# Kernel optimization log

Measured on AMD Instinct MI355X. Metric: run time of the kernel, lower is better.

Reference implementation:

```python
import jax, jax.numpy as jnp
import numpy as np

N, T, D = 2, 4096, 1024
H, E, L = 8, 4, 32
DK, DV = 64, 64

def setup_inputs():
    key = jax.random.key(0)
    ks = jax.random.split(key, 8)
    def randw(k, *d):
        return jax.random.normal(k, d, dtype=jnp.float32) / np.float32(np.sqrt(d[-1]))
    return {
        "X": jax.random.normal(ks[0], (N, T, D), dtype=jnp.float32),
        "w_G": randw(ks[1], H, E, D),
        "b_G": jnp.full((H, E), -float(H) ** 0.5, dtype=jnp.float32),
        "w_K": randw(ks[2], H, DK, D),
        "w_V": randw(ks[3], H, DV, D),
        "w_Q": randw(ks[4], H, DK, D),
        "w_O": randw(ks[5], DV * H, D),
        "init_K_rec": randw(ks[6], E, L, DK),
        "init_V_rec": randw(ks[7], E, L, DV),
    }

def _pscan(A, Xv, Y0):
    # Y_t = A_t * Y_{t-1} + X_t along axis 3 (chunk index), Y_{-1} = Y0
    Ae = jnp.broadcast_to(A[..., None], Xv.shape)
    Xv = Xv.at[..., 0, :].add(A[..., 0, None] * Y0)
    def op(c1, c2):
        a1, x1 = c1
        a2, x2 = c2
        return a1 * a2, a2 * x1 + x2
    _, Y = jax.lax.associative_scan(op, (Ae, Xv), axis=3)
    return Y

def reference(X, w_G, b_G, w_K, w_V, w_Q, w_O, init_K_rec, init_V_rec):
    n, t, _ = X.shape
    t_pad = ((t - 1) // L + 1) * L
    Xp = jnp.pad(X, ((0, 0), (0, t_pad - t), (0, 0)))
    # gates and projections
    G = jax.nn.sigmoid(jnp.einsum('ntd,hed->nhet', Xp, w_G) + b_G[None, :, :, None])
    K = jnp.einsum('ntc,hdc->nhtd', Xp, w_K)
    V = jnp.einsum('ntc,hdc->nhtd', Xp, w_V)
    A = 1.0 - jnp.minimum(G.sum(axis=1), 1.0)               # [n, E, t_pad]
    gK = jnp.einsum('nhet,nhtd->netd', G, K)
    gV = jnp.einsum('nhet,nhtd->netd', G, V)
    # split time as (L, t_pad//L): outer dim L, scan over chunk index (matches torch unflatten(2,(L,-1)))
    tc = t_pad // L
    A = A.reshape(n, E, L, tc)
    gK = gK.reshape(n, E, L, tc, DK)
    gV = gV.reshape(n, E, L, tc, DV)
    iK = jnp.broadcast_to(init_K_rec[None], (n, E, L, DK))
    iV = jnp.broadcast_to(init_V_rec[None], (n, E, L, DV))
    nK = _pscan(A, gK, iK).reshape(n, E, t_pad, DK)
    nV = _pscan(A, gV, iV).reshape(n, E, t_pad, DV)
    recK = jnp.concatenate([iK, nK], axis=2)                 # [n, E, L+t_pad, DK]
    recV = jnp.concatenate([iV, nV], axis=2)
    # moving window of size L ending at current position (slice starts at index 1 of rec buffer)
    idx = 1 + jnp.arange(t_pad)[:, None] + jnp.arange(L)[None, :]
    uk = recK[:, :, idx]                                     # [n, E, t_pad, L, DK]
    uv = recV[:, :, idx]                                     # [n, E, t_pad, L, DV]
    Q = jnp.einsum('ntc,hdc->nhtd', Xp, w_Q)
    scores = jnp.einsum('nhtd,netld->nhtel', Q, uk) / jnp.float32(np.sqrt(DK))
    probs = jax.nn.softmax(scores.reshape(n, H, t_pad, E * L), axis=-1).reshape(scores.shape)
    Y = jnp.einsum('nhtel,netld->nthd', probs, uv).reshape(n, t_pad, H * DV)
    return (Y @ w_O)[:, :t]
```

## Files before the change

### kernel.cpp

```cpp
#include <hip/hip_runtime.h>
#include <hip/hip_bf16.h>


using f4 = float4;
typedef __attribute__((ext_vector_type(8))) short short8;
typedef __attribute__((ext_vector_type(4))) float floatx4;

__device__ __forceinline__ ushort f2bf(float x) {
  unsigned u = __float_as_uint(x);
  u += 0x7fffu + ((u >> 16) & 1u);
  return (ushort)(u >> 16);
}
__device__ __forceinline__ unsigned pk2(float lo, float hi) {
  return (unsigned)f2bf(lo) | ((unsigned)f2bf(hi) << 16);
}
__device__ __forceinline__ float bflo(unsigned pk) { return __uint_as_float(pk << 16); }
__device__ __forceinline__ float bfhi(unsigned pk) { return __uint_as_float(pk & 0xffff0000u); }

__device__ __forceinline__ void gll16(const void* g, void* l) {
  __builtin_amdgcn_global_load_lds((const __attribute__((address_space(1))) void*)g,
                                   (__attribute__((address_space(3))) void*)l, 16, 0, 0);
}

__global__ __launch_bounds__(256)
void conv_f32_bf16(const float* __restrict__ src, ushort* __restrict__ dst, int n4) {
  for (int i = blockIdx.x * blockDim.x + threadIdx.x; i < n4; i += gridDim.x * blockDim.x) {
    f4 v = ((const f4*)src)[i];
    ushort4 o; o.x = f2bf(v.x); o.y = f2bf(v.y); o.z = f2bf(v.z); o.w = f2bf(v.w);
    ((ushort4*)dst)[i] = o;
  }
}

__global__ __launch_bounds__(256)
void conv_weights(const float* __restrict__ wK, const float* __restrict__ wV,
                  const float* __restrict__ wQ, const float* __restrict__ wG,
                  ushort* __restrict__ wAll) {
  int i4 = blockIdx.x * 256 + threadIdx.x;
  int idx = i4 * 4;
  int row = idx >> 10;
  f4 v = make_float4(0.f, 0.f, 0.f, 0.f);
  if (row < 512)       v = *(const f4*)&wK[idx];
  else if (row < 1024) v = *(const f4*)&wV[idx - 524288];
  else if (row < 1536) v = *(const f4*)&wQ[idx - 1048576];
  else if (row < 1568) v = *(const f4*)&wG[idx - 1572864];
  ushort4 o; o.x = f2bf(v.x); o.y = f2bf(v.y); o.z = f2bf(v.z); o.w = f2bf(v.w);
  *(ushort4*)&wAll[idx] = o;
}

__global__ __launch_bounds__(256)
void transpose_wO(const float* __restrict__ wO, ushort* __restrict__ wObf) {
  int i = blockIdx.x * 256 + threadIdx.x;
  int n = i >> 9, k = i & 511;
  wObf[i] = f2bf(wO[(size_t)k * 1024 + n]);
}

__global__ __launch_bounds__(256)
void proj_gemm_mfma(const ushort* __restrict__ Xbf, const ushort* __restrict__ wAll,
                    float* __restrict__ Kp, float* __restrict__ Vp,
                    float* __restrict__ Qp, float* __restrict__ Glin)
{
  __shared__ ushort As[4096];
  __shared__ ushort Bs[4096];
  const int tid = threadIdx.x;
  const int m0 = blockIdx.y * 128;
  const int ct = blockIdx.x;

  float* C; int Nc, n0;
  if (ct < 12) {
    int which = ct >> 2;
    C = (which == 0) ? Kp : (which == 1) ? Vp : Qp;
    Nc = 512; n0 = (ct & 3) * 128;
  } else { C = Glin; Nc = 32; n0 = 0; }

  const int lane = tid & 63;
  const int wv = tid >> 6;
  const int wm = (wv >> 1) * 64, wn = (wv & 1) * 64;

  const int srow = tid >> 2, scol = (tid & 3) * 8;
  const ushort* gA = Xbf  + (size_t)(m0 + srow) * 1024 + scol;
  const ushort* gB = wAll + (size_t)(ct * 128 + srow) * 1024 + scol;
  ushort* lA0 = &As[tid * 8]; ushort* lA1 = &As[2048 + tid * 8];
  ushort* lB0 = &Bs[tid * 8]; ushort* lB1 = &Bs[2048 + tid * 8];

  floatx4 acc[4][4];
#pragma unroll
  for (int i = 0; i < 4; i++)
#pragma unroll
    for (int j = 0; j < 4; j++) acc[i][j] = (floatx4){0.f, 0.f, 0.f, 0.f};

  const int fr = lane & 15;
  const int fk = (lane >> 4) * 8;
  const short8* pA[4]; const short8* pB[4];
#pragma unroll
  for (int i = 0; i < 4; i++) {
    pA[i] = (const short8*)&As[(wm + i * 16 + fr) * 32 + fk];
    pB[i] = (const short8*)&Bs[(wn + i * 16 + fr) * 32 + fk];
  }

  for (int k0 = 0; k0 < 1024; k0 += 32) {
    gll16(gA + k0, lA0);
    gll16(gA + 65536 + k0, lA1);
    gll16(gB + k0, lB0);
    gll16(gB + 65536 + k0, lB1);
    __syncthreads();
    short8 a[4], b[4];
#pragma unroll
    for (int i = 0; i < 4; i++) { a[i] = *pA[i]; b[i] = *pB[i]; }
#pragma unroll
    for (int mi = 0; mi < 4; mi++)
#pragma unroll
      for (int ni = 0; ni < 4; ni++)
        acc[mi][ni] = __builtin_amdgcn_mfma_f32_16x16x32_bf16(a[mi], b[ni], acc[mi][ni], 0, 0, 0);
    __syncthreads();
  }

  const int fq = lane >> 4;
#pragma unroll
  for (int mi = 0; mi < 4; mi++) {
    int row = m0 + wm + mi * 16 + fq * 4;
#pragma unroll
    for (int ni = 0; ni < 4; ni++) {
      int col = n0 + wn + ni * 16 + fr;
      if (col < Nc) {
#pragma unroll
        for (int j = 0; j < 4; j++)
          C[(size_t)(row + j) * Nc + col] = acc[mi][ni][j];
      }
    }
  }
}

__global__ __launch_bounds__(256)
void out_gemm_mfma(const ushort* __restrict__ Ybf, const ushort* __restrict__ wObf,
                   float* __restrict__ out)
{
  __shared__ ushort As[4096];
  __shared__ ushort Bs[4096];
  const int tid = threadIdx.x;
  const int m0 = blockIdx.y * 128;
  const int n0 = blockIdx.x * 128;
  const int lane = tid & 63;
  const int wv = tid >> 6;
  const int wm = (wv >> 1) * 64, wn = (wv & 1) * 64;

  const int srow = tid >> 2, scol = (tid & 3) * 8;
  const ushort* gA = Ybf  + (size_t)(m0 + srow) * 512 + scol;
  const ushort* gB = wObf + (size_t)(n0 + srow) * 512 + scol;
  ushort* lA0 = &As[tid * 8]; ushort* lA1 = &As[2048 + tid * 8];
  ushort* lB0 = &Bs[tid * 8]; ushort* lB1 = &Bs[2048 + tid * 8];

  floatx4 acc[4][4];
#pragma unroll
  for (int i = 0; i < 4; i++)
#pragma unroll
    for (int j = 0; j < 4; j++) acc[i][j] = (floatx4){0.f, 0.f, 0.f, 0.f};

  const int fr = lane & 15;
  const int fk = (lane >> 4) * 8;
  const short8* pA[4]; const short8* pB[4];
#pragma unroll
  for (int i = 0; i < 4; i++) {
    pA[i] = (const short8*)&As[(wm + i * 16 + fr) * 32 + fk];
    pB[i] = (const short8*)&Bs[(wn + i * 16 + fr) * 32 + fk];
  }

  for (int k0 = 0; k0 < 512; k0 += 32) {
    gll16(gA + k0, lA0);
    gll16(gA + 32768 + k0, lA1);
    gll16(gB + k0, lB0);
    gll16(gB + 32768 + k0, lB1);
    __syncthreads();
    short8 a[4], b[4];
#pragma unroll
    for (int i = 0; i < 4; i++) { a[i] = *pA[i]; b[i] = *pB[i]; }
#pragma unroll
    for (int mi = 0; mi < 4; mi++)
#pragma unroll
      for (int ni = 0; ni < 4; ni++)
        acc[mi][ni] = __builtin_amdgcn_mfma_f32_16x16x32_bf16(a[mi], b[ni], acc[mi][ni], 0, 0, 0);
    __syncthreads();
  }

  const int fq = lane >> 4;
#pragma unroll
  for (int mi = 0; mi < 4; mi++) {
    int row = m0 + wm + mi * 16 + fq * 4;
#pragma unroll
    for (int ni = 0; ni < 4; ni++) {
      int col = n0 + wn + ni * 16 + fr;
#pragma unroll
      for (int j = 0; j < 4; j++)
        out[(size_t)(row + j) * 1024 + col] = acc[mi][ni][j];
    }
  }
}

__global__ __launch_bounds__(256)
void gate_kernel(const float* __restrict__ Glin, const float* __restrict__ bG,
                 const float* __restrict__ Kp, const float* __restrict__ Vp,
                 float* __restrict__ gK, float* __restrict__ gV, float* __restrict__ Aout)
{
  const int nt = blockIdx.x * 4 + (threadIdx.x >> 6);
  const int lane = threadIdx.x & 63;
  const int n = nt >> 12;
  const int t = nt & 4095;

  float g[32];
  float gsum[4] = {0.f, 0.f, 0.f, 0.f};
#pragma unroll
  for (int f = 0; f < 32; f++) {
    float z = Glin[(size_t)nt * 32 + f] + bG[f];
    float s = 1.f / (1.f + __expf(-z));
    g[f] = s;
    gsum[f & 3] += s;
  }
  if (lane < 4) {
    float a = 1.f - fminf(gsum[lane], 1.f);
    Aout[(size_t)(n * 4 + lane) * 4096 + t] = a;
  }
  float gk[4] = {0.f, 0.f, 0.f, 0.f}, gv[4] = {0.f, 0.f, 0.f, 0.f};
#pragma unroll
  for (int h = 0; h < 8; h++) {
    float kv = Kp[(size_t)nt * 512 + h * 64 + lane];
    float vv = Vp[(size_t)nt * 512 + h * 64 + lane];
#pragma unroll
    for (int e = 0; e < 4; e++) {
      gk[e] = fmaf(g[h * 4 + e], kv, gk[e]);
      gv[e] = fmaf(g[h * 4 + e], vv, gv[e]);
    }
  }
#pragma unroll
  for (int e = 0; e < 4; e++) {
    size_t base = ((size_t)(n * 4 + e) * 4096 + t) * 64 + lane;
    gK[base] = gk[e];
    gV[base] = gv[e];
  }
}

__global__ __launch_bounds__(64)
void scan_kernel(float* __restrict__ gK, float* __restrict__ gV,
                 const float* __restrict__ Aarr,
                 const float* __restrict__ initK, const float* __restrict__ initV)
{
  __shared__ float sB[128 * 64];
  __shared__ float sA[128];
  const int b = blockIdx.x;
  const int half = b >> 8, sub = b & 255;
  float* gX = half ? gV : gK;
  const float* initX = half ? initV : initK;
  const int n = sub >> 7, r = sub & 127, e = r >> 5, l = r & 31;
  const int tbase = l * 128;
  const size_t base = ((size_t)(n * 4 + e) * 4096 + tbase) * 64;
  const int tid = threadIdx.x;

  const f4* src = (const f4*)&gX[base];
#pragma unroll
  for (int q = 0; q < 32; q++)
    *(f4*)&sB[(tid + q * 64) * 4] = src[tid + q * 64];
  sA[tid]      = Aarr[(size_t)(n * 4 + e) * 4096 + tbase + tid];
  sA[64 + tid] = Aarr[(size_t)(n * 4 + e) * 4096 + tbase + 64 + tid];
  __syncthreads();

  float state = initX[((size_t)e * 32 + l) * 64 + tid];
  float* dst = &gX[base];
  for (int c = 0; c < 128; c++) {
    state = fmaf(sA[c], state, sB[c * 64 + tid]);
    dst[c * 64 + tid] = state;
  }
}

__global__ __launch_bounds__(256, 1)
void attn_mfma(const float* __restrict__ Qp, const float* __restrict__ nK,
               const float* __restrict__ nV, const float* __restrict__ initK,
               const float* __restrict__ initV, ushort* __restrict__ Yout)
{
  __shared__ ushort Kw[4][4096];
  __shared__ ushort Vt[4][4096];
  __shared__ ushort Pl[4][4096];

  const int blk = blockIdx.x;
  const int n = blk >> 7, c = blk & 127;
  const int t0 = c * 32;
  const int tid = threadIdx.x;
  const int lane = tid & 63;
  const int w = tid >> 6;
  const int l15 = lane & 15, lg = lane >> 4;

  short8 qf[4][2];
#pragma unroll
  for (int mi = 0; mi < 4; mi++) {
    int m = w * 64 + mi * 16 + l15;
    int t = t0 + (m & 31), h = m >> 5;
    const float* src = &Qp[((size_t)(n * 4096 + t)) * 512 + h * 64];
#pragma unroll
    for (int kk = 0; kk < 2; kk++) {
      int k = kk * 32 + lg * 8;
      f4 a = *(const f4*)&src[k];
      f4 b = *(const f4*)&src[k + 4];
      short8 v;
      v[0] = (short)f2bf(a.x * 0.125f); v[1] = (short)f2bf(a.y * 0.125f);
      v[2] = (short)f2bf(a.z * 0.125f); v[3] = (short)f2bf(a.w * 0.125f);
      v[4] = (short)f2bf(b.x * 0.125f); v[5] = (short)f2bf(b.y * 0.125f);
      v[6] = (short)f2bf(b.z * 0.125f); v[7] = (short)f2bf(b.w * 0.125f);
      qf[mi][kk] = v;
    }
  }

#pragma unroll 4
  for (int it = 0; it < 16; it++) {
    int idx = it * 256 + tid;
    int e = idx >> 10, u = (idx >> 4) & 63, d = (idx & 15) * 4;
    int s = t0 - 31 + u;
    int scl = s < 4095 ? s : 4095;
    const float* pK = (s >= 0) ? &nK[(((size_t)(n * 4 + e)) * 4096 + scl) * 64 + d]
                               : &initK[((size_t)e * 32 + (s + 32)) * 64 + d];
    const float* pV = (s >= 0) ? &nV[(((size_t)(n * 4 + e)) * 4096 + scl) * 64 + d]
                               : &initV[((size_t)e * 32 + (s + 32)) * 64 + d];
    f4 kv = *(const f4*)pK;
    f4 vv = *(const f4*)pV;
    if (u == 63) { kv = make_float4(0.f,0.f,0.f,0.f); vv = make_float4(0.f,0.f,0.f,0.f); }
    uint2 kp; kp.x = pk2(kv.x, kv.y); kp.y = pk2(kv.z, kv.w);
    int ka = (u * 128 + d * 2) ^ ((u & 7) << 4);
    *(uint2*)((char*)&Kw[e][0] + ka) = kp;
    ushort vb[4] = { f2bf(vv.x), f2bf(vv.y), f2bf(vv.z), f2bf(vv.w) };
#pragma unroll
    for (int q = 0; q < 4; q++) {
      int dq = d + q;
      int va = (dq * 128 + u * 2) ^ ((dq & 7) << 4);
      *(ushort*)((char*)&Vt[e][0] + va) = vb[q];
    }
  }
  __syncthreads();

  floatx4 Yacc[4][4];
#pragma unroll
  for (int mi = 0; mi < 4; mi++)
#pragma unroll
    for (int nd = 0; nd < 4; nd++) Yacc[mi][nd] = (floatx4){0.f,0.f,0.f,0.f};
  float mrun[4][4], lrun[4][4];
#pragma unroll
  for (int mi = 0; mi < 4; mi++)
#pragma unroll
    for (int r = 0; r < 4; r++) { mrun[mi][r] = -1e30f; lrun[mi][r] = 0.f; }

  const floatx4 zf = (floatx4){0.f,0.f,0.f,0.f};
  char* pb = (char*)&Pl[w][0];

#pragma unroll
  for (int half = 0; half < 2; half++) {
    floatx4 S[2][4][4];
#pragma unroll
    for (int ep = 0; ep < 2; ep++) {
      const int e = half * 2 + ep;
#pragma unroll
      for (int ni = 0; ni < 4; ni++) {
        const int urow = ni * 16 + l15;
        const int sw = (urow & 7) << 4;
        short8 kf0 = *(const short8*)((const char*)&Kw[e][0] + ((urow * 128 + lg * 16) ^ sw));
        short8 kf1 = *(const short8*)((const char*)&Kw[e][0] + ((urow * 128 + 64 + lg * 16) ^ sw));
#pragma unroll
        for (int mi = 0; mi < 4; mi++) {
          floatx4 t_ = __builtin_amdgcn_mfma_f32_16x16x32_bf16(qf[mi][0], kf0, zf, 0, 0, 0);
          S[ep][mi][ni] = __builtin_amdgcn_mfma_f32_16x16x32_bf16(qf[mi][1], kf1, t_, 0, 0, 0);
        }
      }
    }
#pragma unroll
    for (int mi = 0; mi < 4; mi++)
#pragma unroll
      for (int r = 0; r < 4; r++) {
        const int iq = (mi & 1) * 16 + lg * 4 + r;
        float mx = mrun[mi][r];
#pragma unroll
        for (int ep = 0; ep < 2; ep++)
#pragma unroll
          for (int ni = 0; ni < 4; ni++) {
            const int u = ni * 16 + l15;
            float v = ((unsigned)(u - iq) < 32u) ? S[ep][mi][ni][r] : -1e30f;
            S[ep][mi][ni][r] = v;
            mx = fmaxf(mx, v);
          }
        mx = fmaxf(mx, __shfl_xor(mx, 1));
        mx = fmaxf(mx, __shfl_xor(mx, 2));
        mx = fmaxf(mx, __shfl_xor(mx, 4));
        mx = fmaxf(mx, __shfl_xor(mx, 8));
        float sc = __expf(mrun[mi][r] - mx);
        mrun[mi][r] = mx;
        float sum = 0.f;
#pragma unroll
        for (int ep = 0; ep < 2; ep++)
#pragma unroll
          for (int ni = 0; ni < 4; ni++) {
            float p = __expf(S[ep][mi][ni][r] - mx);
            S[ep][mi][ni][r] = p;
            sum += p;
          }
        sum += __shfl_xor(sum, 1);
        sum += __shfl_xor(sum, 2);
        sum += __shfl_xor(sum, 4);
        sum += __shfl_xor(sum, 8);
        lrun[mi][r] = lrun[mi][r] * sc + sum;
#pragma unroll
        for (int nd = 0; nd < 4; nd++) Yacc[mi][nd][r] *= sc;
      }
#pragma unroll
    for (int ep = 0; ep < 2; ep++) {
      const int e = half * 2 + ep;
#pragma unroll
      for (int mi = 0; mi < 4; mi++)
#pragma unroll
        for (int r = 0; r < 4; r++) {
          const int m = mi * 16 + lg * 4 + r;
          const int base = m * 128, sw = (m & 7) << 4;
#pragma unroll
          for (int ni = 0; ni < 4; ni++) {
            const int u = ni * 16 + l15;
            *(ushort*)(pb + ((base + u * 2) ^ sw)) = f2bf(S[ep][mi][ni][r]);
          }
        }
      asm volatile("s_waitcnt lgkmcnt(0)" ::: "memory");
      __builtin_amdgcn_sched_barrier(0);
#pragma unroll
      for (int kk = 0; kk < 2; kk++) {
        short8 pa[4];
#pragma unroll
        for (int mi = 0; mi < 4; mi++) {
          const int m = mi * 16 + l15;
          pa[mi] = *(const short8*)(pb + ((m * 128 + kk * 64 + lg * 16) ^ ((m & 7) << 4)));
        }
#pragma unroll
        for (int nd = 0; nd < 4; nd++) {
          const int dr = nd * 16 + l15;
          short8 vf = *(const short8*)((const char*)&Vt[e][0] +
                        ((dr * 128 + kk * 64 + lg * 16) ^ ((dr & 7) << 4)));
#pragma unroll
          for (int mi = 0; mi < 4; mi++)
            Yacc[mi][nd] = __builtin_amdgcn_mfma_f32_16x16x32_bf16(pa[mi], vf, Yacc[mi][nd], 0, 0, 0);
        }
      }
    }
  }

#pragma unroll
  for (int mi = 0; mi < 4; mi++)
#pragma unroll
    for (int r = 0; r < 4; r++) {
      const float inv = 1.f / lrun[mi][r];
      const int m = w * 64 + mi * 16 + lg * 4 + r;
      const int t = t0 + (m & 31), h = m >> 5;
      ushort* dst = &Yout[((size_t)(n * 4096 + t)) * 512 + h * 64];
#pragma unroll
      for (int nd = 0; nd < 4; nd++)
        dst[nd * 16 + l15] = f2bf(Yacc[mi][nd][r] * inv);
    }
}

extern "C" void kernel_launch(void* const* d_in, const int* in_sizes, int n_in,
                              void* d_out, int out_size, void* d_ws, size_t ws_size,
                              hipStream_t stream) {
  const float* X     = (const float*)d_in[0];
  const float* wG    = (const float*)d_in[1];
  const float* bG    = (const float*)d_in[2];
  const float* wK    = (const float*)d_in[3];
  const float* wV    = (const float*)d_in[4];
  const float* wQ    = (const float*)d_in[5];
  const float* wO    = (const float*)d_in[6];
  const float* initK = (const float*)d_in[7];
  const float* initV = (const float*)d_in[8];
  float* out = (float*)d_out;

  float* ws = (float*)d_ws;
  ushort* Xbf  = (ushort*)(ws + 0);
  float*  gK   = ws + 0;
  float*  gV   = ws + 2097152;
  ushort* wAll = (ushort*)(ws + 4194304);
  ushort* wObf = (ushort*)(ws + 5046272);
  float*  Glin = ws + 5308416;
  float*  Kp   = ws + 5570560;
  ushort* Ybf  = (ushort*)Kp;
  float*  Vp   = ws + 9764864;
  float*  Qp   = ws + 13959168;
  float*  Aarr = ws + 18153472;

  conv_f32_bf16<<<2048, 256, 0, stream>>>(X, Xbf, 2097152);
  conv_weights<<<1664, 256, 0, stream>>>(wK, wV, wQ, wG, wAll);
  transpose_wO<<<2048, 256, 0, stream>>>(wO, wObf);
  proj_gemm_mfma<<<dim3(13, 64), 256, 0, stream>>>(Xbf, wAll, Kp, Vp, Qp, Glin);
  gate_kernel<<<2048, 256, 0, stream>>>(Glin, bG, Kp, Vp, gK, gV, Aarr);
  scan_kernel<<<512, 64, 0, stream>>>(gK, gV, Aarr, initK, initV);
  attn_mfma<<<256, 256, 0, stream>>>(Qp, gK, gV, initK, initV, Ybf);
  out_gemm_mfma<<<dim3(8, 64), 256, 0, stream>>>(Ybf, wObf, out);
}
```

Baseline: 226.5 us.

## Rewrite projection GEMM with 256x256 tiles and multi-stage LDS pipeline; emit bf16 Q

Replaces the 128x128 single-buffered projection GEMM with a 512-thread kernel. It computes 256x256 output tiles through a 4-slot LDS ring that prefetches two K-steps ahead, maps blocks to XCDs, and raises wave priority around the MFMA block. The epilogue writes Q already scaled and converted to bf16, so the attention kernel loads bf16 fragments directly instead of converting fp32. Weight packing is padded to 1792 rows to fit whole tiles, which adds some wasted compute on the gate columns. The 128KB of LDS per block limits occupancy to one block per CU.

```diff
diff --git a/kernel.cpp b/kernel.cpp
--- a/kernel.cpp
+++ b/kernel.cpp
@@ -14,8 +14,6 @@
 __device__ __forceinline__ unsigned pk2(float lo, float hi) {
   return (unsigned)f2bf(lo) | ((unsigned)f2bf(hi) << 16);
 }
-__device__ __forceinline__ float bflo(unsigned pk) { return __uint_as_float(pk << 16); }
-__device__ __forceinline__ float bfhi(unsigned pk) { return __uint_as_float(pk & 0xffff0000u); }
 
 __device__ __forceinline__ void gll16(const void* g, void* l) {
   __builtin_amdgcn_global_load_lds((const __attribute__((address_space(1))) void*)g,
@@ -54,77 +52,98 @@
   wObf[i] = f2bf(wO[(size_t)k * 1024 + n]);
 }
 
-__global__ __launch_bounds__(256)
-void proj_gemm_mfma(const ushort* __restrict__ Xbf, const ushort* __restrict__ wAll,
-                    float* __restrict__ Kp, float* __restrict__ Vp,
-                    float* __restrict__ Qp, float* __restrict__ Glin)
+#define PROJ_STEP(KT, WAITS, STAGE_) do {                                        \
+  asm volatile("s_waitcnt vmcnt(" WAITS ")" ::: "memory");                       \
+  __builtin_amdgcn_s_barrier();                                                  \
+  asm volatile("" ::: "memory");                                                 \
+  if (STAGE_) {                                                                  \
+    const int k2 = ((KT) + 2) * 32;                                              \
+    ushort* la = &As[(((KT) + 2) & 3) * 8192 + tid * 8];                         \
+    ushort* lb = &Bs[(((KT) + 2) & 3) * 8192 + tid * 8];                         \
+    gll16(gA + k2, la); gll16(gA + 131072 + k2, la + 4096);                      \
+    gll16(gB + k2, lb); gll16(gB + 131072 + k2, lb + 4096);                      \
+  }                                                                              \
+  {                                                                              \
+    const int ko = ((KT) & 3) * 8192;                                            \
+    short8 bfrag[4];                                                             \
+    _Pragma("unroll")                                                            \
+    for (int ni = 0; ni < 4; ni++)                                               \
+      bfrag[ni] = *(const short8*)(Bf + ko + ni * 512);                          \
+    __builtin_amdgcn_s_setprio(1);                                               \
+    _Pragma("unroll")                                                            \
+    for (int mi = 0; mi < 8; mi++) {                                             \
+      short8 afrag = *(const short8*)(Af + ko + mi * 512);                       \
+      _Pragma("unroll")                                                          \
+      for (int ni = 0; ni < 4; ni++)                                             \
+        acc[mi][ni] = __builtin_amdgcn_mfma_f32_16x16x32_bf16(                   \
+            afrag, bfrag[ni], acc[mi][ni], 0, 0, 0);                             \
+    }                                                                            \
+    __builtin_amdgcn_s_setprio(0);                                               \
+  }                                                                              \
+} while (0)
+
+__global__ __launch_bounds__(512, 2)
+void proj_gemm_256(const ushort* __restrict__ Xbf, const ushort* __restrict__ wAll,
+                   float* __restrict__ Kp, float* __restrict__ Vp,
+                   ushort* __restrict__ Qbf, float* __restrict__ Glin)
 {
-  __shared__ ushort As[4096];
-  __shared__ ushort Bs[4096];
+  __shared__ ushort As[4 * 8192];
+  __shared__ ushort Bs[4 * 8192];
+
   const int tid = threadIdx.x;
-  const int m0 = blockIdx.y * 128;
-  const int ct = blockIdx.x;
-
-  float* C; int Nc, n0;
-  if (ct < 12) {
-    int which = ct >> 2;
-    C = (which == 0) ? Kp : (which == 1) ? Vp : Qp;
-    Nc = 512; n0 = (ct & 3) * 128;
-  } else { C = Glin; Nc = 32; n0 = 0; }
+  const int bid = blockIdx.x;
+  const int xcd = bid & 7, slot = bid >> 3;
+  const int ct = slot % 7;
+  const int my = xcd * 4 + slot / 7;
+  const int m0 = my * 256;
+  const int n0 = ct * 256;
 
   const int lane = tid & 63;
-  const int wv = tid >> 6;
-  const int wm = (wv >> 1) * 64, wn = (wv & 1) * 64;
-
-  const int srow = tid >> 2, scol = (tid & 3) * 8;
-  const ushort* gA = Xbf  + (size_t)(m0 + srow) * 1024 + scol;
-  const ushort* gB = wAll + (size_t)(ct * 128 + srow) * 1024 + scol;
-  ushort* lA0 = &As[tid * 8]; ushort* lA1 = &As[2048 + tid * 8];
-  ushort* lB0 = &Bs[tid * 8]; ushort* lB1 = &Bs[2048 + tid * 8];
-
-  floatx4 acc[4][4];
-#pragma unroll
-  for (int i = 0; i < 4; i++)
-#pragma unroll
-    for (int j = 0; j < 4; j++) acc[i][j] = (floatx4){0.f, 0.f, 0.f, 0.f};
-
-  const int fr = lane & 15;
-  const int fk = (lane >> 4) * 8;
-  const short8* pA[4]; const short8* pB[4];
-#pragma unroll
-  for (int i = 0; i < 4; i++) {
-    pA[i] = (const short8*)&As[(wm + i * 16 + fr) * 32 + fk];
-    pB[i] = (const short8*)&Bs[(wn + i * 16 + fr) * 32 + fk];
-  }
-
-  for (int k0 = 0; k0 < 1024; k0 += 32) {
-    gll16(gA + k0, lA0);
-    gll16(gA + 65536 + k0, lA1);
-    gll16(gB + k0, lB0);
-    gll16(gB + 65536 + k0, lB1);
-    __syncthreads();
-    short8 a[4], b[4];
-#pragma unroll
-    for (int i = 0; i < 4; i++) { a[i] = *pA[i]; b[i] = *pB[i]; }
-#pragma unroll
-    for (int mi = 0; mi < 4; mi++)
-#pragma unroll
-      for (int ni = 0; ni < 4; ni++)
-        acc[mi][ni] = __builtin_amdgcn_mfma_f32_16x16x32_bf16(a[mi], b[ni], acc[mi][ni], 0, 0, 0);
-    __syncthreads();
-  }
-
-  const int fq = lane >> 4;
-#pragma unroll
-  for (int mi = 0; mi < 4; mi++) {
-    int row = m0 + wm + mi * 16 + fq * 4;
+  const int w = tid >> 6;
+  const int wm = (w >> 2) * 128;
+  const int wn = (w & 3) * 64;
+  const int l15 = lane & 15, lg = lane >> 4;
+
+  const int srow = tid >> 2, sc8 = (tid & 3) * 8;
+  const ushort* gA = Xbf  + (size_t)(m0 + srow) * 1024 + sc8;
+  const ushort* gB = wAll + (size_t)(n0 + srow) * 1024 + sc8;
+
+  const ushort* Af = As + (wm + l15) * 32 + lg * 8;
+  const ushort* Bf = Bs + (wn + l15) * 32 + lg * 8;
+
+  floatx4 acc[8][4];
+#pragma unroll
+  for (int mi = 0; mi < 8; mi++)
+#pragma unroll
+    for (int ni = 0; ni < 4; ni++) acc[mi][ni] = (floatx4){0.f, 0.f, 0.f, 0.f};
+
+#pragma unroll
+  for (int t_ = 0; t_ < 2; t_++) {
+    const int k0 = t_ * 32;
+    ushort* la = &As[t_ * 8192 + tid * 8];
+    ushort* lb = &Bs[t_ * 8192 + tid * 8];
+    gll16(gA + k0, la); gll16(gA + 131072 + k0, la + 4096);
+    gll16(gB + k0, lb); gll16(gB + 131072 + k0, lb + 4096);
+  }
+
+#pragma unroll 1
+  for (int kt = 0; kt < 30; ++kt) PROJ_STEP(kt, "4", true);
+  PROJ_STEP(30, "4", false);
+  PROJ_STEP(31, "0", false);
+
+#pragma unroll
+  for (int mi = 0; mi < 8; mi++) {
+    const int rm = m0 + wm + mi * 16 + lg * 4;
 #pragma unroll
     for (int ni = 0; ni < 4; ni++) {
-      int col = n0 + wn + ni * 16 + fr;
-      if (col < Nc) {
-#pragma unroll
-        for (int j = 0; j < 4; j++)
-          C[(size_t)(row + j) * Nc + col] = acc[mi][ni][j];
+      const int cn = wn + ni * 16 + l15;
+#pragma unroll
+      for (int j = 0; j < 4; j++) {
+        const float v = acc[mi][ni][j];
+        if (ct < 2)      Kp [(size_t)(rm + j) * 512 + ct * 256 + cn] = v;
+        else if (ct < 4) Vp [(size_t)(rm + j) * 512 + (ct - 2) * 256 + cn] = v;
+        else if (ct < 6) Qbf[(size_t)(rm + j) * 512 + (ct - 4) * 256 + cn] = f2bf(v * 0.125f);
+        else if (cn < 32) Glin[(size_t)(rm + j) * 32 + cn] = v;
       }
     }
   }
@@ -184,13 +203,13 @@
   const int fq = lane >> 4;
 #pragma unroll
   for (int mi = 0; mi < 4; mi++) {
-    int row = m0 + wm + mi * 16 + fq * 4;
+    int rm = m0 + wm + mi * 16 + fq * 4;
 #pragma unroll
     for (int ni = 0; ni < 4; ni++) {
-      int col = n0 + wn + ni * 16 + fr;
+      int cn = n0 + wn + ni * 16 + fr;
 #pragma unroll
       for (int j = 0; j < 4; j++)
-        out[(size_t)(row + j) * 1024 + col] = acc[mi][ni][j];
+        out[(size_t)(rm + j) * 1024 + cn] = acc[mi][ni][j];
     }
   }
 }
@@ -270,7 +289,7 @@
 }
 
 __global__ __launch_bounds__(256, 1)
-void attn_mfma(const float* __restrict__ Qp, const float* __restrict__ nK,
+void attn_mfma(const ushort* __restrict__ Qbf, const float* __restrict__ nK,
                const float* __restrict__ nV, const float* __restrict__ initK,
                const float* __restrict__ initV, ushort* __restrict__ Yout)
 {
@@ -291,19 +310,10 @@
   for (int mi = 0; mi < 4; mi++) {
     int m = w * 64 + mi * 16 + l15;
     int t = t0 + (m & 31), h = m >> 5;
-    const float* src = &Qp[((size_t)(n * 4096 + t)) * 512 + h * 64];
-#pragma unroll
-    for (int kk = 0; kk < 2; kk++) {
-      int k = kk * 32 + lg * 8;
-      f4 a = *(const f4*)&src[k];
-      f4 b = *(const f4*)&src[k + 4];
-      short8 v;
-      v[0] = (short)f2bf(a.x * 0.125f); v[1] = (short)f2bf(a.y * 0.125f);
-      v[2] = (short)f2bf(a.z * 0.125f); v[3] = (short)f2bf(a.w * 0.125f);
-      v[4] = (short)f2bf(b.x * 0.125f); v[5] = (short)f2bf(b.y * 0.125f);
-      v[6] = (short)f2bf(b.z * 0.125f); v[7] = (short)f2bf(b.w * 0.125f);
-      qf[mi][kk] = v;
-    }
+    const ushort* src = &Qbf[((size_t)(n * 4096 + t)) * 512 + h * 64];
+#pragma unroll
+    for (int kk = 0; kk < 2; kk++)
+      qf[mi][kk] = *(const short8*)&src[kk * 32 + lg * 8];
   }
 
 #pragma unroll 4
@@ -474,20 +484,20 @@
   float*  gK   = ws + 0;
   float*  gV   = ws + 2097152;
   ushort* wAll = (ushort*)(ws + 4194304);
-  ushort* wObf = (ushort*)(ws + 5046272);
-  float*  Glin = ws + 5308416;
-  float*  Kp   = ws + 5570560;
+  ushort* wObf = (ushort*)(ws + 5111808);
+  float*  Glin = ws + 5373952;
+  float*  Kp   = ws + 5636096;
   ushort* Ybf  = (ushort*)Kp;
-  float*  Vp   = ws + 9764864;
-  float*  Qp   = ws + 13959168;
-  float*  Aarr = ws + 18153472;
+  float*  Vp   = ws + 9830400;
+  ushort* Qbf  = (ushort*)(ws + 14024704);
+  float*  Aarr = ws + 16121856;
 
   conv_f32_bf16<<<2048, 256, 0, stream>>>(X, Xbf, 2097152);
-  conv_weights<<<1664, 256, 0, stream>>>(wK, wV, wQ, wG, wAll);
+  conv_weights<<<1792, 256, 0, stream>>>(wK, wV, wQ, wG, wAll);
   transpose_wO<<<2048, 256, 0, stream>>>(wO, wObf);
-  proj_gemm_mfma<<<dim3(13, 64), 256, 0, stream>>>(Xbf, wAll, Kp, Vp, Qp, Glin);
+  proj_gemm_256<<<224, 512, 0, stream>>>(Xbf, wAll, Kp, Vp, Qbf, Glin);
   gate_kernel<<<2048, 256, 0, stream>>>(Glin, bG, Kp, Vp, gK, gV, Aarr);
   scan_kernel<<<512, 64, 0, stream>>>(gK, gV, Aarr, initK, initV);
-  attn_mfma<<<256, 256, 0, stream>>>(Qp, gK, gV, initK, initV, Ybf);
+  attn_mfma<<<256, 256, 0, stream>>>(Qbf, gK, gV, initK, initV, Ybf);
   out_gemm_mfma<<<dim3(8, 64), 256, 0, stream>>>(Ybf, wObf, out);
 }
```

After: 222.9 us. No clear change (-1.6%).

## Emit pre-scaled bf16 Q from projection GEMM and remap blocks per XCD

Applied to the files above, without the earlier changes.

The projection GEMM now writes Q as bf16 already scaled by 1/sqrt(dk), so the attention kernel loads short8 fragments directly instead of reading fp32 and converting. This halves Q write and read traffic. The projection grid becomes 1D with an XCD-aware swizzle that keeps each XCD on a contiguous band of M rows for L2 reuse of X. Both GEMMs also get a min-blocks-per-CU hint of 4, which may constrain register allocation.

```diff
diff --git a/kernel.cpp b/kernel.cpp
--- a/kernel.cpp
+++ b/kernel.cpp
@@ -14,8 +14,6 @@
 __device__ __forceinline__ unsigned pk2(float lo, float hi) {
   return (unsigned)f2bf(lo) | ((unsigned)f2bf(hi) << 16);
 }
-__device__ __forceinline__ float bflo(unsigned pk) { return __uint_as_float(pk << 16); }
-__device__ __forceinline__ float bfhi(unsigned pk) { return __uint_as_float(pk & 0xffff0000u); }
 
 __device__ __forceinline__ void gll16(const void* g, void* l) {
   __builtin_amdgcn_global_load_lds((const __attribute__((address_space(1))) void*)g,
@@ -54,31 +52,28 @@
   wObf[i] = f2bf(wO[(size_t)k * 1024 + n]);
 }
 
-__global__ __launch_bounds__(256)
-void proj_gemm_mfma(const ushort* __restrict__ Xbf, const ushort* __restrict__ wAll,
-                    float* __restrict__ Kp, float* __restrict__ Vp,
-                    float* __restrict__ Qp, float* __restrict__ Glin)
+__global__ __launch_bounds__(256, 4)
+void proj_gemm_m97(const ushort* __restrict__ Xbf, const ushort* __restrict__ wAll,
+                   float* __restrict__ Kp, float* __restrict__ Vp,
+                   ushort* __restrict__ Qbf, float* __restrict__ Glin)
 {
   __shared__ ushort As[4096];
   __shared__ ushort Bs[4096];
+
   const int tid = threadIdx.x;
-  const int m0 = blockIdx.y * 128;
-  const int ct = blockIdx.x;
-
-  float* C; int Nc, n0;
-  if (ct < 12) {
-    int which = ct >> 2;
-    C = (which == 0) ? Kp : (which == 1) ? Vp : Qp;
-    Nc = 512; n0 = (ct & 3) * 128;
-  } else { C = Glin; Nc = 32; n0 = 0; }
-
-  const int lane = tid & 63;
-  const int wv = tid >> 6;
-  const int wm = (wv >> 1) * 64, wn = (wv & 1) * 64;
+  const int bid = blockIdx.x;
+  const int xcd = bid & 7, slot = bid >> 3;
+  const int ct = slot % 13;
+  const int my = xcd * 8 + slot / 13;
+  const int m0 = my * 128, n0 = ct * 128;
+
+  const int lane = tid & 63, w = tid >> 6;
+  const int wm = (w >> 1) * 64, wn = (w & 1) * 64;
+  const int l15 = lane & 15, lg = lane >> 4;
 
   const int srow = tid >> 2, scol = (tid & 3) * 8;
   const ushort* gA = Xbf  + (size_t)(m0 + srow) * 1024 + scol;
-  const ushort* gB = wAll + (size_t)(ct * 128 + srow) * 1024 + scol;
+  const ushort* gB = wAll + (size_t)(n0 + srow) * 1024 + scol;
   ushort* lA0 = &As[tid * 8]; ushort* lA1 = &As[2048 + tid * 8];
   ushort* lB0 = &Bs[tid * 8]; ushort* lB1 = &Bs[2048 + tid * 8];
 
@@ -88,13 +83,11 @@
 #pragma unroll
     for (int j = 0; j < 4; j++) acc[i][j] = (floatx4){0.f, 0.f, 0.f, 0.f};
 
-  const int fr = lane & 15;
-  const int fk = (lane >> 4) * 8;
   const short8* pA[4]; const short8* pB[4];
 #pragma unroll
   for (int i = 0; i < 4; i++) {
-    pA[i] = (const short8*)&As[(wm + i * 16 + fr) * 32 + fk];
-    pB[i] = (const short8*)&Bs[(wn + i * 16 + fr) * 32 + fk];
+    pA[i] = (const short8*)&As[(wm + i * 16 + l15) * 32 + lg * 8];
+    pB[i] = (const short8*)&Bs[(wn + i * 16 + l15) * 32 + lg * 8];
   }
 
   for (int k0 = 0; k0 < 1024; k0 += 32) {
@@ -114,23 +107,25 @@
     __syncthreads();
   }
 
-  const int fq = lane >> 4;
 #pragma unroll
   for (int mi = 0; mi < 4; mi++) {
-    int row = m0 + wm + mi * 16 + fq * 4;
+    const int rm = m0 + wm + mi * 16 + lg * 4;
 #pragma unroll
     for (int ni = 0; ni < 4; ni++) {
-      int col = n0 + wn + ni * 16 + fr;
-      if (col < Nc) {
-#pragma unroll
-        for (int j = 0; j < 4; j++)
-          C[(size_t)(row + j) * Nc + col] = acc[mi][ni][j];
+      const int Cg = n0 + wn + ni * 16 + l15;
+#pragma unroll
+      for (int j = 0; j < 4; j++) {
+        const float v = acc[mi][ni][j];
+        if (Cg < 512)        Kp [(size_t)(rm + j) * 512 + Cg] = v;
+        else if (Cg < 1024)  Vp [(size_t)(rm + j) * 512 + Cg - 512] = v;
+        else if (Cg < 1536)  Qbf[(size_t)(rm + j) * 512 + Cg - 1024] = f2bf(v * 0.125f);
+        else if (Cg < 1568)  Glin[(size_t)(rm + j) * 32 + Cg - 1536] = v;
       }
     }
   }
 }
 
-__global__ __launch_bounds__(256)
+__global__ __launch_bounds__(256, 4)
 void out_gemm_mfma(const ushort* __restrict__ Ybf, const ushort* __restrict__ wObf,
                    float* __restrict__ out)
 {
@@ -184,13 +179,13 @@
   const int fq = lane >> 4;
 #pragma unroll
   for (int mi = 0; mi < 4; mi++) {
-    int row = m0 + wm + mi * 16 + fq * 4;
+    int rm = m0 + wm + mi * 16 + fq * 4;
 #pragma unroll
     for (int ni = 0; ni < 4; ni++) {
-      int col = n0 + wn + ni * 16 + fr;
+      int cn = n0 + wn + ni * 16 + fr;
 #pragma unroll
       for (int j = 0; j < 4; j++)
-        out[(size_t)(row + j) * 1024 + col] = acc[mi][ni][j];
+        out[(size_t)(rm + j) * 1024 + cn] = acc[mi][ni][j];
     }
   }
 }
@@ -270,7 +265,7 @@
 }
 
 __global__ __launch_bounds__(256, 1)
-void attn_mfma(const float* __restrict__ Qp, const float* __restrict__ nK,
+void attn_mfma(const ushort* __restrict__ Qbf, const float* __restrict__ nK,
                const float* __restrict__ nV, const float* __restrict__ initK,
                const float* __restrict__ initV, ushort* __restrict__ Yout)
 {
@@ -291,19 +286,10 @@
   for (int mi = 0; mi < 4; mi++) {
     int m = w * 64 + mi * 16 + l15;
     int t = t0 + (m & 31), h = m >> 5;
-    const float* src = &Qp[((size_t)(n * 4096 + t)) * 512 + h * 64];
-#pragma unroll
-    for (int kk = 0; kk < 2; kk++) {
-      int k = kk * 32 + lg * 8;
-      f4 a = *(const f4*)&src[k];
-      f4 b = *(const f4*)&src[k + 4];
-      short8 v;
-      v[0] = (short)f2bf(a.x * 0.125f); v[1] = (short)f2bf(a.y * 0.125f);
-      v[2] = (short)f2bf(a.z * 0.125f); v[3] = (short)f2bf(a.w * 0.125f);
-      v[4] = (short)f2bf(b.x * 0.125f); v[5] = (short)f2bf(b.y * 0.125f);
-      v[6] = (short)f2bf(b.z * 0.125f); v[7] = (short)f2bf(b.w * 0.125f);
-      qf[mi][kk] = v;
-    }
+    const ushort* src = &Qbf[((size_t)(n * 4096 + t)) * 512 + h * 64];
+#pragma unroll
+    for (int kk = 0; kk < 2; kk++)
+      qf[mi][kk] = *(const short8*)&src[kk * 32 + lg * 8];
   }
 
 #pragma unroll 4
@@ -474,20 +460,20 @@
   float*  gK   = ws + 0;
   float*  gV   = ws + 2097152;
   ushort* wAll = (ushort*)(ws + 4194304);
-  ushort* wObf = (ushort*)(ws + 5046272);
-  float*  Glin = ws + 5308416;
-  float*  Kp   = ws + 5570560;
+  ushort* wObf = (ushort*)(ws + 5111808);
+  float*  Glin = ws + 5373952;
+  float*  Kp   = ws + 5636096;
   ushort* Ybf  = (ushort*)Kp;
-  float*  Vp   = ws + 9764864;
-  float*  Qp   = ws + 13959168;
-  float*  Aarr = ws + 18153472;
+  float*  Vp   = ws + 9830400;
+  ushort* Qbf  = (ushort*)(ws + 14024704);
+  float*  Aarr = ws + 16121856;
 
   conv_f32_bf16<<<2048, 256, 0, stream>>>(X, Xbf, 2097152);
   conv_weights<<<1664, 256, 0, stream>>>(wK, wV, wQ, wG, wAll);
   transpose_wO<<<2048, 256, 0, stream>>>(wO, wObf);
-  proj_gemm_mfma<<<dim3(13, 64), 256, 0, stream>>>(Xbf, wAll, Kp, Vp, Qp, Glin);
+  proj_gemm_m97<<<832, 256, 0, stream>>>(Xbf, wAll, Kp, Vp, Qbf, Glin);
   gate_kernel<<<2048, 256, 0, stream>>>(Glin, bG, Kp, Vp, gK, gV, Aarr);
   scan_kernel<<<512, 64, 0, stream>>>(gK, gV, Aarr, initK, initV);
-  attn_mfma<<<256, 256, 0, stream>>>(Qp, gK, gV, initK, initV, Ybf);
+  attn_mfma<<<256, 256, 0, stream>>>(Qbf, gK, gV, initK, initV, Ybf);
   out_gemm_mfma<<<dim3(8, 64), 256, 0, stream>>>(Ybf, wObf, out);
 }
```

New measurement: 209.9 us. -7.3%, faster.
